# Optimization experiments

Measured on AMD Instinct MI355X. Metric: run time of the kernel, lower is better.

Reference implementation:

```python
import jax, jax.numpy as jnp
import numpy as np

N_STATE = 64
N_LAYERS = 4
D_MODEL = 512
D_OUT = 256
BATCH = 16
SEQLEN = 2048


def setup_inputs() -> dict:
    key = jax.random.key(0)
    ks = jax.random.split(key, 16)
    H, N, nl = D_MODEL, N_STATE, N_LAYERS
    inp = {}
    inp["x"] = jax.random.normal(ks[0], (BATCH, SEQLEN, D_MODEL), dtype=jnp.float32)
    # encoder / decoder dense
    inp["enc_w"] = jax.random.normal(ks[1], (D_MODEL, D_MODEL), jnp.float32) / np.sqrt(D_MODEL)
    inp["enc_b"] = jnp.zeros((D_MODEL,), jnp.float32)
    inp["dec_w"] = jax.random.normal(ks[2], (D_MODEL, D_OUT), jnp.float32) / np.sqrt(D_MODEL)
    inp["dec_b"] = jnp.zeros((D_OUT,), jnp.float32)
    # per-layer LayerNorm
    inp["ln_scale"] = jnp.ones((nl, D_MODEL), jnp.float32)
    inp["ln_bias"] = jnp.zeros((nl, D_MODEL), jnp.float32)
    # per-layer S4 DPLR params (stored as real/imag float pairs)
    inp["lambda_re"] = -0.5 * jnp.ones((nl, H, N), jnp.float32)
    inp["lambda_im"] = jnp.broadcast_to(np.pi * jnp.arange(N, dtype=jnp.float32), (nl, H, N))
    inp["p_re"] = jax.random.normal(ks[3], (nl, H, N), jnp.float32) * 0.5
    inp["p_im"] = jax.random.normal(ks[4], (nl, H, N), jnp.float32) * 0.5
    inp["b_re"] = jax.random.normal(ks[5], (nl, H, N), jnp.float32) * 0.5
    inp["b_im"] = jax.random.normal(ks[6], (nl, H, N), jnp.float32) * 0.5
    inp["c_re"] = jax.random.normal(ks[7], (nl, H, N), jnp.float32) * 0.5
    inp["c_im"] = jax.random.normal(ks[8], (nl, H, N), jnp.float32) * 0.5
    inp["log_step"] = jax.random.uniform(ks[9], (nl, H), jnp.float32, minval=np.log(1e-3), maxval=np.log(1e-1))
    inp["d_param"] = jnp.ones((nl, H), jnp.float32)
    # per-layer output Dense
    inp["out_w"] = jax.random.normal(ks[10], (nl, D_MODEL, D_MODEL), jnp.float32) / np.sqrt(D_MODEL)
    inp["out_b"] = jnp.zeros((nl, D_MODEL), jnp.float32)
    return inp


def _layer_norm(x, scale, bias, eps=1e-6):
    mu = jnp.mean(x, axis=-1, keepdims=True)
    var = jnp.mean(jnp.square(x - mu), axis=-1, keepdims=True)
    return (x - mu) * jax.lax.rsqrt(var + eps) * scale + bias


def _kernel_dplr(Lam, P, B, C, step, L):
    # Lam,P,B,C: [H,N] complex64; step: [H] float32 -> K: [H,L] float32
    theta = (2.0 * np.pi / L) * jnp.arange(L, dtype=jnp.float32)
    Omega = jnp.exp(-1j * theta)                        # [L] roots of unity
    g = (2.0 / step)[:, None] * ((1.0 - Omega) / (1.0 + Omega))[None, :]  # [H,L]
    c = 2.0 / (1.0 + Omega)                             # [L]
    r = 1.0 / (g[:, :, None] - Lam[:, None, :])         # [H,L,N] resolvent (Cauchy)
    Cc, Pc = jnp.conj(C), jnp.conj(P)
    k00 = jnp.einsum("hn,hln->hl", Cc * B, r)
    k01 = jnp.einsum("hn,hln->hl", Cc * P, r)
    k10 = jnp.einsum("hn,hln->hl", Pc * B, r)
    k11 = jnp.einsum("hn,hln->hl", Pc * P, r)
    at_roots = c[None, :] * (k00 - k01 * (1.0 / (1.0 + k11)) * k10)  # [H,L]
    return jnp.fft.ifft(at_roots, n=L, axis=-1).real


def _s4_apply(u, Lam, P, B, C, step, D):
    # u: [Bt,L,H]; causal FFT convolution with kernel K[h,:] per channel
    L = u.shape[1]
    K = _kernel_dplr(Lam, P, B, C, step, L)             # [H,L]
    ud = jnp.fft.rfft(u, n=2 * L, axis=1)               # [Bt,L+1,H]
    Kd = jnp.fft.rfft(K, n=2 * L, axis=-1)              # [H,L+1]
    y = jnp.fft.irfft(ud * Kd.T[None], n=2 * L, axis=1)[:, :L]
    return y + D[None, None, :] * u


def reference(x, enc_w, enc_b, ln_scale, ln_bias, lambda_re, lambda_im,
              p_re, p_im, b_re, b_im, c_re, c_im, log_step, d_param,
              out_w, out_b, dec_w, dec_b):
    h = x @ enc_w + enc_b
    n_layers = ln_scale.shape[0]
    for i in range(n_layers):
        skip = h
        z = _layer_norm(h, ln_scale[i], ln_bias[i])
        Lam = lambda_re[i] + 1j * lambda_im[i]
        P = p_re[i] + 1j * p_im[i]
        B = b_re[i] + 1j * b_im[i]
        C = c_re[i] + 1j * c_im[i]
        z = _s4_apply(z, Lam, P, B, C, jnp.exp(log_step[i]), d_param[i])
        z = jax.nn.gelu(z)
        z = z @ out_w[i] + out_b[i]
        h = skip + z  # dropout=0.0 -> identity
    logits = h @ dec_w + dec_b
    return jax.nn.log_softmax(logits, axis=-1)
```

## Files before the change

### kernel.cpp

```cpp
#include <hip/hip_runtime.h>
#include <hip/hip_bf16.h>

#define NLAY 4
#define DH   512
#define NST  64
#define NB   16
#define SL   2048
#define NDO  256
#define BL   (NB*SL)
#define KDIM 512
#define TWOPI 6.283185307179586476925287

typedef unsigned short u16;
typedef __attribute__((ext_vector_type(8))) short  short8v;
typedef __attribute__((ext_vector_type(8))) unsigned short ushort8v;
typedef __attribute__((ext_vector_type(4))) float  f32x4;

#define RCPF(x) __builtin_amdgcn_rcpf(x)

__device__ __forceinline__ float bf2f(u16 v){
  union { unsigned u; float f; } x; x.u = ((unsigned)v) << 16; return x.f;
}
__device__ __forceinline__ u16 f2bf(float f){
  union { float f; unsigned u; } x; x.f = f;
  unsigned u = x.u;
  unsigned r = u + 0x7fffu + ((u >> 16) & 1u);
  return (u16)(r >> 16);
}
__device__ __forceinline__ void cmulw(float& xr, float& xi, float wr, float wi){
  float tr = xr*wr - xi*wi;
  xi = fmaf(xr, wi, xi*wr);
  xr = tr;
}
__device__ __forceinline__ float gelu_fast(float v){
  const float c0 = 0.7978845608028654f;
  float u = c0 * fmaf(0.044715f, v*v*v, v);
  return v * RCPF(1.0f + __expf(-2.0f * u));
}

template<int SGN>
__device__ __forceinline__ void dft4w(float& r0, float& i0, float& r1, float& i1,
                                      float& r2, float& i2, float& r3, float& i3){
  const float t0r = r0 + r2, t0i = i0 + i2;
  const float t1r = r0 - r2, t1i = i0 - i2;
  const float t2r = r1 + r3, t2i = i1 + i3;
  const float t3r = r1 - r3, t3i = i1 - i3;
  r0 = t0r + t2r; i0 = t0i + t2i;
  r2 = t0r - t2r; i2 = t0i - t2i;
  if (SGN < 0){ r1 = t1r + t3i; i1 = t1i - t3r; r3 = t1r - t3i; i3 = t1i + t3r; }
  else        { r1 = t1r - t3i; i1 = t1i + t3r; r3 = t1r + t3i; i3 = t1i - t3r; }
}

template<int SGN>
__device__ __forceinline__ void dft16(float* re, float* im){
#pragma unroll
  for (int b = 0; b < 4; b++)
    dft4w<SGN>(re[b], im[b], re[4+b], im[4+b], re[8+b], im[8+b], re[12+b], im[12+b]);
  const float C1 = 0.92387953251128675613f, S1_ = 0.38268343236508977172f;
  const float C2 = 0.70710678118654752440f;
  const float sg = (SGN < 0) ? -1.f : 1.f;
  cmulw(re[5],  im[5],   C1,  sg*S1_);
  cmulw(re[9],  im[9],   C2,  sg*C2);
  cmulw(re[13], im[13],  S1_, sg*C1);
  cmulw(re[6],  im[6],   C2,  sg*C2);
  cmulw(re[10], im[10],  0.f, sg*1.f);
  cmulw(re[14], im[14], -C2,  sg*C2);
  cmulw(re[7],  im[7],   S1_, sg*C1);
  cmulw(re[11], im[11], -C2,  sg*C2);
  cmulw(re[15], im[15], -C1,  sg*(-S1_));
#pragma unroll
  for (int c = 0; c < 4; c++)
    dft4w<SGN>(re[4*c], im[4*c], re[4*c+1], im[4*c+1], re[4*c+2], im[4*c+2], re[4*c+3], im[4*c+3]);
  float tr_, ti_;
#define SWP(A,B) tr_=re[A]; re[A]=re[B]; re[B]=tr_; ti_=im[A]; im[A]=im[B]; im[B]=ti_;
  SWP(1,4) SWP(2,8) SWP(3,12) SWP(6,9) SWP(7,13) SWP(11,14)
#undef SWP
}

__device__ __forceinline__ int cxpad(int i){ return i + (i >> 4) + ((i >> 8) << 1); }
#define CXSZ 4384

__device__ __forceinline__ void fwd4096(float* re, float* im, float2* cx, int t){
  dft16<-1>(re, im);
  const float a0 = -(float)(TWOPI/4096.0) * (float)t;
#pragma unroll
  for (int k = 0; k < 16; k++){
    if (k){ float sn = __sinf(a0*(float)k), cs = __cosf(a0*(float)k); cmulw(re[k], im[k], cs, sn); }
    cx[cxpad(t + 256*k)] = make_float2(re[k], im[k]);
  }
  __syncthreads();
  const int k1 = t >> 4, m2 = t & 15;
  const int b2 = k1*256 + m2;
#pragma unroll
  for (int j = 0; j < 16; j++){ float2 v = cx[cxpad(b2 + 16*j)]; re[j] = v.x; im[j] = v.y; }
  dft16<-1>(re, im);
  const float b0 = -(float)(TWOPI/256.0) * (float)m2;
  __syncthreads();
#pragma unroll
  for (int k = 0; k < 16; k++){
    if (k){ float sn = __sinf(b0*(float)k), cs = __cosf(b0*(float)k); cmulw(re[k], im[k], cs, sn); }
    cx[cxpad(b2 + 16*k)] = make_float2(re[k], im[k]);
  }
  __syncthreads();
#pragma unroll
  for (int j = 0; j < 16; j++){ float2 v = cx[cxpad(16*t + j)]; re[j] = v.x; im[j] = v.y; }
  dft16<-1>(re, im);
}

__device__ __forceinline__ void inv4096(float* re, float* im, float2* cx, int t){
  dft16<1>(re, im);
#pragma unroll
  for (int j = 0; j < 16; j++) cx[cxpad(16*t + j)] = make_float2(re[j], im[j]);
  __syncthreads();
  const int k1 = t >> 4, m2 = t & 15;
  const int b2 = k1*256 + m2;
  const float b0 = (float)(TWOPI/256.0) * (float)m2;
#pragma unroll
  for (int k = 0; k < 16; k++){
    float2 v = cx[cxpad(b2 + 16*k)];
    re[k] = v.x; im[k] = v.y;
    if (k){ float sn = __sinf(b0*(float)k), cs = __cosf(b0*(float)k); cmulw(re[k], im[k], cs, sn); }
  }
  dft16<1>(re, im);
  __syncthreads();
#pragma unroll
  for (int j = 0; j < 16; j++) cx[cxpad(b2 + 16*j)] = make_float2(re[j], im[j]);
  __syncthreads();
  const float a0 = (float)(TWOPI/4096.0) * (float)t;
#pragma unroll
  for (int k = 0; k < 16; k++){
    float2 v = cx[cxpad(t + 256*k)];
    re[k] = v.x; im[k] = v.y;
    if (k){ float sn = __sinf(a0*(float)k), cs = __cosf(a0*(float)k); cmulw(re[k], im[k], cs, sn); }
  }
  dft16<1>(re, im);
}

__global__ __launch_bounds__(256) void prep_k(
  const float* __restrict__ lam_re, const float* __restrict__ lam_im,
  const float* __restrict__ p_re,  const float* __restrict__ p_im,
  const float* __restrict__ b_re,  const float* __restrict__ b_im,
  const float* __restrict__ c_re,  const float* __restrict__ c_im,
  float4* __restrict__ cwA, float4* __restrict__ cwB, float* __restrict__ cwS)
{
  const int i = blockIdx.x * 256 + threadIdx.x;
  const float lr = lam_re[i], li = lam_im[i];
  const float pr = p_re[i],  pi = p_im[i];
  const float br = b_re[i],  bi = b_im[i];
  const float cr = c_re[i],  ci = c_im[i];
  cwA[i] = make_float4(lr, li, cr*br + ci*bi, cr*bi - ci*br);
  cwB[i] = make_float4(cr*pr + ci*pi, cr*pi - ci*pr, pr*br + pi*bi, pr*bi - pi*br);
  cwS[i] = pr*pr + pi*pi;
}

__global__ __launch_bounds__(256, 2) void cauchy_k(
    const float4* __restrict__ cwA, const float4* __restrict__ cwB,
    const float* __restrict__ cwS, const float* __restrict__ lstep,
    float2* __restrict__ Kd)
{
  const int t = threadIdx.x;
  const int h = blockIdx.y, lay = blockIdx.z;
  const int lb = blockIdx.x * 256 + t;
  const int wb = (lay*DH + h) * NST;
  const float tw0 = 2.0f * expf(-lstep[lay*DH + h]);

  float T0,T1,T2,T3, g0,g1,g2,g3;
  { float sn, cs;
    sincosf((float)(TWOPI/4096.0)*(float)(lb       ), &sn, &cs); T0 = sn*RCPF(cs); g0 = tw0*T0;
    sincosf((float)(TWOPI/4096.0)*(float)(lb +  512), &sn, &cs); T1 = sn*RCPF(cs); g1 = tw0*T1;
    sincosf((float)(TWOPI/4096.0)*(float)(lb + 1024), &sn, &cs); T2 = sn*RCPF(cs); g2 = tw0*T2;
    sincosf((float)(TWOPI/4096.0)*(float)(lb + 1536), &sn, &cs); T3 = sn*RCPF(cs); g3 = tw0*T3;
  }

  float k00r0=0,k00i0=0,k01r0=0,k01i0=0,k10r0=0,k10i0=0,k11r0=0,k11i0=0;
  float k00r1=0,k00i1=0,k01r1=0,k01i1=0,k10r1=0,k10i1=0,k11r1=0,k11i1=0;
  float k00r2=0,k00i2=0,k01r2=0,k01i2=0,k10r2=0,k10i2=0,k11r2=0,k11i2=0;
  float k00r3=0,k00i3=0,k01r3=0,k01i3=0,k10r3=0,k10i3=0,k11r3=0,k11i3=0;

  for (int n = 0; n < NST; n++){
    const float4 A  = cwA[wb + n];
    const float4 Bv = cwB[wb + n];
    const float w11 = cwS[wb + n];
    const float nlr = -A.x;
    const float dr2 = A.x * A.x;
#define CSTEP(J) { \
    const float di = g##J - A.y; \
    const float sI = RCPF(fmaf(di, di, dr2)); \
    const float ivr = nlr * sI, ivi = -di * sI; \
    k00r##J = fmaf(A.z,  ivr, fmaf(-A.w,  ivi, k00r##J)); \
    k00i##J = fmaf(A.z,  ivi, fmaf( A.w,  ivr, k00i##J)); \
    k01r##J = fmaf(Bv.x, ivr, fmaf(-Bv.y, ivi, k01r##J)); \
    k01i##J = fmaf(Bv.x, ivi, fmaf( Bv.y, ivr, k01i##J)); \
    k10r##J = fmaf(Bv.z, ivr, fmaf(-Bv.w, ivi, k10r##J)); \
    k10i##J = fmaf(Bv.z, ivi, fmaf( Bv.w, ivr, k10i##J)); \
    k11r##J = fmaf(w11,  ivr, k11r##J); \
    k11i##J = fmaf(w11,  ivi, k11i##J); }
    CSTEP(0) CSTEP(1) CSTEP(2) CSTEP(3)
#undef CSTEP
  }

  float2* kp = Kd + (size_t)(lay*DH + h) * 4096;
#define COUT(J, LOFF) { \
    const float d1r = 1.f + k11r##J, d1i = k11i##J; \
    const float idn = RCPF(fmaf(d1r, d1r, d1i*d1i)); \
    const float wr = k01r##J*k10r##J - k01i##J*k10i##J; \
    const float wi = k01r##J*k10i##J + k01i##J*k10r##J; \
    const float vr = fmaf(wr, d1r,  wi*d1i) * idn; \
    const float vi = fmaf(wi, d1r, -wr*d1i) * idn; \
    const float sr = k00r##J - vr, si = k00i##J - vi; \
    kp[lb + LOFF] = make_float2(fmaf(-T##J, si, sr), fmaf(T##J, sr, si)); }
  COUT(0, 0) COUT(1, 512) COUT(2, 1024) COUT(3, 1536)
#undef COUT
}

__global__ __launch_bounds__(256) void kdfft_k(float2* __restrict__ Kd){
  __shared__ float  ar[SL], ai[SL];
  __shared__ float2 cx[CXSZ];
  const int t = threadIdx.x;
  const size_t base = (size_t)blockIdx.x * 4096;
#pragma unroll
  for (int q = 0; q < 8; q++){
    const int l = t + 256*q;
    float2 v = Kd[base + l];
    const int brv = __brev((unsigned)l) >> 21;
    ar[brv] = v.x; ai[brv] = v.y;
  }
  __syncthreads();

  for (int s = 0; s < 11; s++){
    const int half = 1 << s;
    const float fac = (float)(TWOPI) / (float)(2 << s);
#pragma unroll
    for (int q = 0; q < 4; q++){
      const int v = t + 256*q;
      const int pos = v & (half - 1);
      const int i0 = ((v >> s) << (s+1)) + pos;
      const int i1 = i0 + half;
      const float ang = fac * (float)pos;
      const float wc = __cosf(ang), ws = __sinf(ang);
      const float xr = ar[i1], xi = ai[i1];
      const float tr = wc*xr - ws*xi, ti = fmaf(wc, xi, ws*xr);
      const float ur_ = ar[i0], ui_ = ai[i0];
      ar[i0] = ur_ + tr; ai[i0] = ui_ + ti;
      ar[i1] = ur_ - tr; ai[i1] = ui_ - ti;
    }
    __syncthreads();
  }

  float re[16], im[16];
#pragma unroll
  for (int j = 0; j < 16; j++){
    re[j] = (j < 8) ? ar[t + 256*j] * (1.0f/2048.f) : 0.f;
    im[j] = 0.f;
  }
  fwd4096(re, im, cx, t);
  float2* kp = Kd + base + 16*t;
#pragma unroll
  for (int k = 0; k < 16; k += 2)
    *(float4*)(kp + k) = make_float4(re[k], im[k], re[k+1], im[k+1]);
}

__global__ __launch_bounds__(256) void wconv_k(const float* __restrict__ src,
    u16* __restrict__ dst, int K, int N){
  __shared__ u16 tile[64][72];
  const size_t mb = (size_t)blockIdx.z * K * N;
  const int k0 = blockIdx.x * 64, n0 = blockIdx.y * 64;
  const int r = threadIdx.x >> 2, c4 = (threadIdx.x & 3) * 16;
  const float* s = src + mb + (size_t)(k0 + r) * N + n0 + c4;
  float4 f0 = *(const float4*)s, f1 = *(const float4*)(s+4);
  float4 f2 = *(const float4*)(s+8), f3 = *(const float4*)(s+12);
  tile[c4+0][r]=f2bf(f0.x); tile[c4+1][r]=f2bf(f0.y); tile[c4+2][r]=f2bf(f0.z); tile[c4+3][r]=f2bf(f0.w);
  tile[c4+4][r]=f2bf(f1.x); tile[c4+5][r]=f2bf(f1.y); tile[c4+6][r]=f2bf(f1.z); tile[c4+7][r]=f2bf(f1.w);
  tile[c4+8][r]=f2bf(f2.x); tile[c4+9][r]=f2bf(f2.y); tile[c4+10][r]=f2bf(f2.z); tile[c4+11][r]=f2bf(f2.w);
  tile[c4+12][r]=f2bf(f3.x); tile[c4+13][r]=f2bf(f3.y); tile[c4+14][r]=f2bf(f3.z); tile[c4+15][r]=f2bf(f3.w);
  __syncthreads();
  u16* d = dst + mb + (size_t)(n0 + r) * K + k0 + c4;
  *(ushort8v*)d       = *(const ushort8v*)&tile[r][c4];
  *(ushort8v*)(d + 8) = *(const ushort8v*)&tile[r][c4 + 8];
}

#define LTILE 32
__device__ __forceinline__ int lnswz(int h){ return ((h >> 1) + (h >> 6)) & 3; }

__global__ __launch_bounds__(256) void lnt_k(const float* __restrict__ hsrc,
    const float* __restrict__ gam, const float* __restrict__ bet,
    u16* __restrict__ zT){
  __shared__ u16 tile[DH][LTILE];
  __shared__ float smu[LTILE], srs[LTILE];
  const int t = threadIdx.x;
  const int b = blockIdx.y, l0 = blockIdx.x * LTILE;
  const int r = t >> 3, hb = (t & 7) * 64;
  const float* p = hsrc + ((size_t)b * SL + l0 + r) * DH + hb;
  float s = 0.f, sq = 0.f;
#pragma unroll
  for (int j4 = 0; j4 < 16; j4++){
    float4 v = *(const float4*)(p + j4*4);
    s  += (v.x + v.y) + (v.z + v.w);
    sq += v.x*v.x + v.y*v.y + v.z*v.z + v.w*v.w;
    const int h0 = hb + j4*4;
    tile[h0+0][r ^ (lnswz(h0+0) << 3)] = f2bf(v.x);
    tile[h0+1][r ^ (lnswz(h0+1) << 3)] = f2bf(v.y);
    tile[h0+2][r ^ (lnswz(h0+2) << 3)] = f2bf(v.z);
    tile[h0+3][r ^ (lnswz(h0+3) << 3)] = f2bf(v.w);
  }
  s  += __shfl_xor(s, 1);  sq += __shfl_xor(sq, 1);
  s  += __shfl_xor(s, 2);  sq += __shfl_xor(sq, 2);
  s  += __shfl_xor(s, 4);  sq += __shfl_xor(sq, 4);
  if ((t & 7) == 0){
    const float mu = s * (1.0f/DH);
    smu[r] = mu;
    srs[r] = rsqrtf(sq * (1.0f/DH) - mu*mu + 1e-6f);
  }
  __syncthreads();

#pragma unroll
  for (int hh = 0; hh < 2; hh++){
    const int h = t + hh*256;
    const float g = gam[h], be = bet[h];
    const int sw = lnswz(h);
    u16* dst = zT + ((size_t)b * DH + h) * SL + l0;
#pragma unroll
    for (int og = 0; og < 4; og++){
      const int lg = og ^ sw;
      ushort8v v = *(const ushort8v*)&tile[h][og*8];
      const float4 m0 = *(const float4*)&smu[lg*8];
      const float4 m1 = *(const float4*)&smu[lg*8 + 4];
      const float4 r0 = *(const float4*)&srs[lg*8];
      const float4 r1 = *(const float4*)&srs[lg*8 + 4];
      ushort8v o;
      o[0] = f2bf(fmaf(bf2f((u16)v[0]) - m0.x, r0.x*g, be));
      o[1] = f2bf(fmaf(bf2f((u16)v[1]) - m0.y, r0.y*g, be));
      o[2] = f2bf(fmaf(bf2f((u16)v[2]) - m0.z, r0.z*g, be));
      o[3] = f2bf(fmaf(bf2f((u16)v[3]) - m0.w, r0.w*g, be));
      o[4] = f2bf(fmaf(bf2f((u16)v[4]) - m1.x, r1.x*g, be));
      o[5] = f2bf(fmaf(bf2f((u16)v[5]) - m1.y, r1.y*g, be));
      o[6] = f2bf(fmaf(bf2f((u16)v[6]) - m1.z, r1.z*g, be));
      o[7] = f2bf(fmaf(bf2f((u16)v[7]) - m1.w, r1.w*g, be));
      *(ushort8v*)(dst + lg*8) = o;
    }
  }
}

__global__ __launch_bounds__(256) void s4conv_k(
    const u16* __restrict__ zT, const float2* __restrict__ Kd,
    const float* __restrict__ dpar, u16* __restrict__ yT)
{
  __shared__ float2 cx[CXSZ];
  const int t = threadIdx.x;
  const int wg = blockIdx.x;
  const int h = wg & 511, bp = wg >> 9;
  const u16* r1 = zT + ((size_t)(2*bp) * DH + h) * SL;
  const u16* r2 = r1 + (size_t)DH * SL;
  float ur1[8], ur2[8];
  float re[16], im[16];
#pragma unroll
  for (int j = 0; j < 8; j++){
    ur1[j] = bf2f(r1[t + 256*j]);
    ur2[j] = bf2f(r2[t + 256*j]);
    re[j] = ur1[j]; im[j] = ur2[j];
  }
#pragma unroll
  for (int j = 8; j < 16; j++){ re[j] = 0.f; im[j] = 0.f; }

  fwd4096(re, im, cx, t);

  const float2* kp = Kd + (size_t)h * 4096 + 16*t;
#pragma unroll
  for (int k = 0; k < 16; k += 2){
    float4 w2 = *(const float4*)(kp + k);
    cmulw(re[k],   im[k],   w2.x, w2.y);
    cmulw(re[k+1], im[k+1], w2.z, w2.w);
  }

  inv4096(re, im, cx, t);

  const float Dv = dpar[h];
  u16* y1 = yT + ((size_t)(2*bp) * DH + h) * SL;
  u16* y2 = y1 + (size_t)DH * SL;
#pragma unroll
  for (int j = 0; j < 8; j++){
    float v1 = fmaf(re[j], (1.0f/4096.f), Dv * ur1[j]);
    float v2 = fmaf(im[j], (1.0f/4096.f), Dv * ur2[j]);
    y1[t + 256*j] = f2bf(gelu_fast(v1));
    y2[t + 256*j] = f2bf(gelu_fast(v2));
  }
}

template<int AMODE, bool RESID>
__global__ __launch_bounds__(256) void gemm_k(
    const void* __restrict__ Aptr, const u16* __restrict__ Wt,
    const float* __restrict__ bias,
    const float* __restrict__ resid, float* __restrict__ Cout,
    int Mb, int N)
{
  __shared__ u16 As[128][40];
  __shared__ u16 Bs[128][40];
  const int t = threadIdx.x;
  const int n0 = blockIdx.x * 128, m0 = blockIdx.y * 128, bb = blockIdx.z;
  const int lane = t & 63, wv = t >> 6;
  const int wm = (wv >> 1) * 64, wn = (wv & 1) * 64;
  f32x4 acc[4][4];
#pragma unroll
  for (int mi = 0; mi < 4; mi++)
#pragma unroll
    for (int ni = 0; ni < 4; ni++) acc[mi][ni] = {0.f, 0.f, 0.f, 0.f};

  const u16*  Ab = (const u16*)Aptr;
  const float* Af = (const float*)Aptr;
  const size_t Abase = (AMODE == 1) ? (size_t)bb * KDIM * Mb : 0;

  for (int k0 = 0; k0 < KDIM; k0 += 32){
    __syncthreads();
    if (AMODE == 1){
      const int kk = t >> 3, ch = t & 7;
      const u16* srca = Ab + Abase + (size_t)(k0 + kk) * Mb + m0 + ch*16;
      ushort8v v0 = *(const ushort8v*)srca;
      ushort8v v1 = *(const ushort8v*)(srca + 8);
      const int col = (kk & 7) | (((kk >> 3) ^ (ch & 3)) << 3);
#pragma unroll
      for (int i = 0; i < 8; i++){
        As[ch*16 + i][col]     = (u16)v0[i];
        As[ch*16 + 8 + i][col] = (u16)v1[i];
      }
    } else if (AMODE == 0){
      const int r = t >> 1, kh = (t & 1) << 4;
      const u16* srca = Ab + (size_t)(m0 + r) * KDIM + k0 + kh;
      ushort8v v0 = *(const ushort8v*)srca;
      ushort8v v1 = *(const ushort8v*)(srca + 8);
      const int s3 = (r >> 4) & 3;
      const int c0 = (((kh >> 3) ^ s3) << 3);
      const int c1 = ((((kh >> 3) + 1) ^ s3) << 3);
      *(ushort8v*)&As[r][c0] = v0;
      *(ushort8v*)&As[r][c1] = v1;
    } else {
      const int r = t >> 1, kh = (t & 1) << 4;
      const float* sf = Af + (size_t)(m0 + r) * KDIM + k0 + kh;
      float4 f0 = *(const float4*)sf,     f1 = *(const float4*)(sf + 4);
      float4 f2 = *(const float4*)(sf+8), f3 = *(const float4*)(sf + 12);
      ushort8v v0, v1;
      v0[0]=f2bf(f0.x); v0[1]=f2bf(f0.y); v0[2]=f2bf(f0.z); v0[3]=f2bf(f0.w);
      v0[4]=f2bf(f1.x); v0[5]=f2bf(f1.y); v0[6]=f2bf(f1.z); v0[7]=f2bf(f1.w);
      v1[0]=f2bf(f2.x); v1[1]=f2bf(f2.y); v1[2]=f2bf(f2.z); v1[3]=f2bf(f2.w);
      v1[4]=f2bf(f3.x); v1[5]=f2bf(f3.y); v1[6]=f2bf(f3.z); v1[7]=f2bf(f3.w);
      const int s3 = (r >> 4) & 3;
      const int c0 = (((kh >> 3) ^ s3) << 3);
      const int c1 = ((((kh >> 3) + 1) ^ s3) << 3);
      *(ushort8v*)&As[r][c0] = v0;
      *(ushort8v*)&As[r][c1] = v1;
    }
    {
      const int r = t >> 1, kh = (t & 1) << 4;
      const u16* srcb = Wt + (size_t)(n0 + r) * KDIM + k0 + kh;
      ushort8v v0 = *(const ushort8v*)srcb;
      ushort8v v1 = *(const ushort8v*)(srcb + 8);
      const int s3 = (r >> 4) & 3;
      const int c0 = (((kh >> 3) ^ s3) << 3);
      const int c1 = ((((kh >> 3) + 1) ^ s3) << 3);
      *(ushort8v*)&Bs[r][c0] = v0;
      *(ushort8v*)&Bs[r][c1] = v1;
    }
    __syncthreads();

    const int ko = (lane >> 4) * 8;
    const int fr = lane & 15;
    short8v af[4], bf[4];
#pragma unroll
    for (int mi = 0; mi < 4; mi++){
      const int col = (((ko >> 3) ^ (((wm >> 4) + mi) & 3)) << 3);
      af[mi] = *(const short8v*)&As[wm + mi*16 + fr][col];
    }
#pragma unroll
    for (int ni = 0; ni < 4; ni++){
      const int col = (((ko >> 3) ^ (((wn >> 4) + ni) & 3)) << 3);
      bf[ni] = *(const short8v*)&Bs[wn + ni*16 + fr][col];
    }
#pragma unroll
    for (int mi = 0; mi < 4; mi++)
#pragma unroll
      for (int ni = 0; ni < 4; ni++)
        acc[mi][ni] = __builtin_amdgcn_mfma_f32_16x16x32_bf16(af[mi], bf[ni], acc[mi][ni], 0, 0, 0);
  }

  const int fr = lane & 15;
  const int rq = (lane >> 4) * 4;
#pragma unroll
  for (int mi = 0; mi < 4; mi++){
#pragma unroll
    for (int ni = 0; ni < 4; ni++){
      const int gn = n0 + wn + ni*16 + fr;
      const float bs = bias[gn];
#pragma unroll
      for (int q = 0; q < 4; q++){
        const int gm = m0 + wm + mi*16 + rq + q;
        const size_t idx = ((size_t)bb * Mb + gm) * N + gn;
        float v = acc[mi][ni][q] + bs;
        if (RESID) v += resid[idx];
        Cout[idx] = v;
      }
    }
  }
}

__global__ __launch_bounds__(256) void lsm_k(float* __restrict__ o){
  const int row = blockIdx.x * 4 + (threadIdx.x >> 6);
  const int lane = threadIdx.x & 63;
  float* p = o + (size_t)row * NDO + lane * 4;
  float4 v = *(const float4*)p;
  float mx = fmaxf(fmaxf(v.x, v.y), fmaxf(v.z, v.w));
#pragma unroll
  for (int q = 32; q; q >>= 1) mx = fmaxf(mx, __shfl_xor(mx, q));
  float e = __expf(v.x - mx) + __expf(v.y - mx) + __expf(v.z - mx) + __expf(v.w - mx);
#pragma unroll
  for (int q = 32; q; q >>= 1) e += __shfl_xor(e, q);
  const float lse = mx + __logf(e);
  v.x -= lse; v.y -= lse; v.z -= lse; v.w -= lse;
  *(float4*)p = v;
}

extern "C" void kernel_launch(void* const* d_in, const int* in_sizes, int n_in,
                              void* d_out, int out_size, void* d_ws, size_t ws_size,
                              hipStream_t stream)
{
  (void)in_sizes; (void)n_in; (void)out_size; (void)ws_size;
  const float* x      = (const float*)d_in[0];
  const float* enc_w  = (const float*)d_in[1];
  const float* enc_b  = (const float*)d_in[2];
  const float* dec_w  = (const float*)d_in[3];
  const float* dec_b  = (const float*)d_in[4];
  const float* ln_s   = (const float*)d_in[5];
  const float* ln_b   = (const float*)d_in[6];
  const float* lam_re = (const float*)d_in[7];
  const float* lam_im = (const float*)d_in[8];
  const float* p_re   = (const float*)d_in[9];
  const float* p_im   = (const float*)d_in[10];
  const float* b_re   = (const float*)d_in[11];
  const float* b_im   = (const float*)d_in[12];
  const float* c_re   = (const float*)d_in[13];
  const float* c_im   = (const float*)d_in[14];
  const float* lstep  = (const float*)d_in[15];
  const float* d_par  = (const float*)d_in[16];
  const float* out_w  = (const float*)d_in[17];
  const float* out_b  = (const float*)d_in[18];

  char* ws = (char*)d_ws;
  float*  hbuf = (float*)(ws);
  u16*    zT   = (u16*)  (ws + (size_t)67108864 + 33554432);
  u16*    yT   = (u16*)  (ws + (size_t)67108864 + 2*33554432);
  float2* Kd   = (float2*)(ws + (size_t)67108864 + 3*33554432);
  u16*    Wt   = (u16*)  (ws + (size_t)67108864 + 3*33554432 + 67108864);
  u16*    WtEnc = Wt;
  u16*    WtOut = Wt + 262144;
  u16*    WtDec = Wt + 262144*5;
  float*  outp = (float*)d_out;

  float4* cwA = (float4*)d_out;
  float4* cwB = cwA + 131072;
  float*  cwS = (float*)(cwB + 131072);

  prep_k<<<dim3(NLAY*DH*NST/256), 256, 0, stream>>>(lam_re, lam_im, p_re, p_im,
                                                    b_re, b_im, c_re, c_im, cwA, cwB, cwS);
  wconv_k<<<dim3(8, 8, 1), 256, 0, stream>>>(enc_w, WtEnc, KDIM, DH);
  wconv_k<<<dim3(8, 8, NLAY), 256, 0, stream>>>(out_w, WtOut, KDIM, DH);
  wconv_k<<<dim3(8, 4, 1), 256, 0, stream>>>(dec_w, WtDec, KDIM, NDO);
  cauchy_k<<<dim3(2, DH, NLAY), 256, 0, stream>>>(cwA, cwB, cwS, lstep, Kd);
  kdfft_k<<<dim3(NLAY*DH), 256, 0, stream>>>(Kd);
  gemm_k<2,false><<<dim3(DH/128, BL/128, 1), 256, 0, stream>>>(
      x, WtEnc, enc_b, nullptr, hbuf, BL, DH);
  for (int i = 0; i < NLAY; i++){
    lnt_k<<<dim3(SL/LTILE, NB), 256, 0, stream>>>(hbuf, ln_s + i*DH, ln_b + i*DH, zT);
    s4conv_k<<<dim3((NB/2)*DH), 256, 0, stream>>>(
        zT, Kd + (size_t)i*DH*4096, d_par + i*DH, yT);
    gemm_k<1,true><<<dim3(DH/128, SL/128, NB), 256, 0, stream>>>(
        yT, WtOut + (size_t)i*262144, out_b + i*DH, hbuf, hbuf, SL, DH);
  }
  gemm_k<2,false><<<dim3(NDO/128, BL/128, 1), 256, 0, stream>>>(
      hbuf, WtDec, dec_b, nullptr, outp, BL, NDO);
  lsm_k<<<dim3(BL/4), 256, 0, stream>>>(outp);
}
```

Baseline: 830.6 us.

## Store residual stream in bf16, trim FFT barriers, unroll Cauchy loop

```diff
diff --git a/kernel.cpp b/kernel.cpp
--- a/kernel.cpp
+++ b/kernel.cpp
@@ -95,7 +95,6 @@
   for (int j = 0; j < 16; j++){ float2 v = cx[cxpad(b2 + 16*j)]; re[j] = v.x; im[j] = v.y; }
   dft16<-1>(re, im);
   const float b0 = -(float)(TWOPI/256.0) * (float)m2;
-  __syncthreads();
 #pragma unroll
   for (int k = 0; k < 16; k++){
     if (k){ float sn = __sinf(b0*(float)k), cs = __cosf(b0*(float)k); cmulw(re[k], im[k], cs, sn); }
@@ -122,7 +121,6 @@
     if (k){ float sn = __sinf(b0*(float)k), cs = __cosf(b0*(float)k); cmulw(re[k], im[k], cs, sn); }
   }
   dft16<1>(re, im);
-  __syncthreads();
 #pragma unroll
   for (int j = 0; j < 16; j++) cx[cxpad(b2 + 16*j)] = make_float2(re[j], im[j]);
   __syncthreads();
@@ -177,6 +175,7 @@
   float k00r2=0,k00i2=0,k01r2=0,k01i2=0,k10r2=0,k10i2=0,k11r2=0,k11i2=0;
   float k00r3=0,k00i3=0,k01r3=0,k01i3=0,k10r3=0,k10i3=0,k11r3=0,k11i3=0;
 
+#pragma unroll 2
   for (int n = 0; n < NST; n++){
     const float4 A  = cwA[wb + n];
     const float4 Bv = cwB[wb + n];
@@ -197,6 +196,8 @@
     k11i##J = fmaf(w11,  ivi, k11i##J); }
     CSTEP(0) CSTEP(1) CSTEP(2) CSTEP(3)
 #undef CSTEP
+    asm volatile("" : "+v"(k00r0), "+v"(k00r1), "+v"(k00r2), "+v"(k00r3),
+                      "+v"(k11i0), "+v"(k11i1), "+v"(k11i2), "+v"(k11i3));
   }
 
   float2* kp = Kd + (size_t)(lay*DH + h) * 4096;
@@ -282,7 +283,7 @@
 #define LTILE 32
 __device__ __forceinline__ int lnswz(int h){ return ((h >> 1) + (h >> 6)) & 3; }
 
-__global__ __launch_bounds__(256) void lnt_k(const float* __restrict__ hsrc,
+__global__ __launch_bounds__(256) void lnt_k(const u16* __restrict__ hsrc,
     const float* __restrict__ gam, const float* __restrict__ bet,
     u16* __restrict__ zT){
   __shared__ u16 tile[DH][LTILE];
@@ -290,18 +291,18 @@
   const int t = threadIdx.x;
   const int b = blockIdx.y, l0 = blockIdx.x * LTILE;
   const int r = t >> 3, hb = (t & 7) * 64;
-  const float* p = hsrc + ((size_t)b * SL + l0 + r) * DH + hb;
+  const u16* p = hsrc + ((size_t)b * SL + l0 + r) * DH + hb;
   float s = 0.f, sq = 0.f;
 #pragma unroll
-  for (int j4 = 0; j4 < 16; j4++){
-    float4 v = *(const float4*)(p + j4*4);
-    s  += (v.x + v.y) + (v.z + v.w);
-    sq += v.x*v.x + v.y*v.y + v.z*v.z + v.w*v.w;
-    const int h0 = hb + j4*4;
-    tile[h0+0][r ^ (lnswz(h0+0) << 3)] = f2bf(v.x);
-    tile[h0+1][r ^ (lnswz(h0+1) << 3)] = f2bf(v.y);
-    tile[h0+2][r ^ (lnswz(h0+2) << 3)] = f2bf(v.z);
-    tile[h0+3][r ^ (lnswz(h0+3) << 3)] = f2bf(v.w);
+  for (int j8 = 0; j8 < 8; j8++){
+    ushort8v w = *(const ushort8v*)(p + j8*8);
+    const int h0 = hb + j8*8;
+#pragma unroll
+    for (int d = 0; d < 8; d++){
+      const float f = bf2f((u16)w[d]);
+      s += f; sq = fmaf(f, f, sq);
+      tile[h0+d][r ^ (lnswz(h0+d) << 3)] = (u16)w[d];
+    }
   }
   s  += __shfl_xor(s, 1);  sq += __shfl_xor(sq, 1);
   s  += __shfl_xor(s, 2);  sq += __shfl_xor(sq, 2);
@@ -386,11 +387,11 @@
   }
 }
 
-template<int AMODE, bool RESID>
+template<int AMODE, bool RESID, bool OUTBF>
 __global__ __launch_bounds__(256) void gemm_k(
     const void* __restrict__ Aptr, const u16* __restrict__ Wt,
     const float* __restrict__ bias,
-    const float* __restrict__ resid, float* __restrict__ Cout,
+    const u16* __restrict__ resid, void* __restrict__ Coutv,
     int Mb, int N)
 {
   __shared__ u16 As[128][40];
@@ -494,8 +495,9 @@
         const int gm = m0 + wm + mi*16 + rq + q;
         const size_t idx = ((size_t)bb * Mb + gm) * N + gn;
         float v = acc[mi][ni][q] + bs;
-        if (RESID) v += resid[idx];
-        Cout[idx] = v;
+        if (RESID) v += bf2f(resid[idx]);
+        if (OUTBF) ((u16*)Coutv)[idx] = f2bf(v);
+        else       ((float*)Coutv)[idx] = v;
       }
     }
   }
@@ -543,7 +545,7 @@
   const float* out_b  = (const float*)d_in[18];
 
   char* ws = (char*)d_ws;
-  float*  hbuf = (float*)(ws);
+  u16*    hbuf = (u16*)(ws);
   u16*    zT   = (u16*)  (ws + (size_t)67108864 + 33554432);
   u16*    yT   = (u16*)  (ws + (size_t)67108864 + 2*33554432);
   float2* Kd   = (float2*)(ws + (size_t)67108864 + 3*33554432);
@@ -564,16 +566,16 @@
   wconv_k<<<dim3(8, 4, 1), 256, 0, stream>>>(dec_w, WtDec, KDIM, NDO);
   cauchy_k<<<dim3(2, DH, NLAY), 256, 0, stream>>>(cwA, cwB, cwS, lstep, Kd);
   kdfft_k<<<dim3(NLAY*DH), 256, 0, stream>>>(Kd);
-  gemm_k<2,false><<<dim3(DH/128, BL/128, 1), 256, 0, stream>>>(
+  gemm_k<2,false,true><<<dim3(DH/128, BL/128, 1), 256, 0, stream>>>(
       x, WtEnc, enc_b, nullptr, hbuf, BL, DH);
   for (int i = 0; i < NLAY; i++){
     lnt_k<<<dim3(SL/LTILE, NB), 256, 0, stream>>>(hbuf, ln_s + i*DH, ln_b + i*DH, zT);
     s4conv_k<<<dim3((NB/2)*DH), 256, 0, stream>>>(
         zT, Kd + (size_t)i*DH*4096, d_par + i*DH, yT);
-    gemm_k<1,true><<<dim3(DH/128, SL/128, NB), 256, 0, stream>>>(
+    gemm_k<1,true,true><<<dim3(DH/128, SL/128, NB), 256, 0, stream>>>(
         yT, WtOut + (size_t)i*262144, out_b + i*DH, hbuf, hbuf, SL, DH);
   }
-  gemm_k<2,false><<<dim3(NDO/128, BL/128, 1), 256, 0, stream>>>(
+  gemm_k<0,false,false><<<dim3(NDO/128, BL/128, 1), 256, 0, stream>>>(
       hbuf, WtDec, dec_b, nullptr, outp, BL, NDO);
   lsm_k<<<dim3(BL/4), 256, 0, stream>>>(outp);
 }
```

Result: faster. 780.1 us (-6.1%).
